# Kernel tuning notes

Hardware: AMD Instinct MI355X
Metric: run time of the kernel (lower is better)

The kernel has to match this reference:

```python
import jax, jax.numpy as jnp
import numpy as np
import math

B, S, D, H = 2, 2048, 512, 8  # batch, seq, d_hidden (= per-head dim here), n_heads


def _rope(x):
    # x: [B, H, S, D]; standard interleaved RoPE with base 10000
    b, h, s, d = x.shape
    inv_freq = 1.0 / (10000.0 ** (jnp.arange(0, d, 2, dtype=jnp.float32) / d))  # [d/2]
    ang = jnp.arange(s, dtype=jnp.float32)[:, None] * inv_freq[None, :]          # [S, d/2]
    cos, sin = jnp.cos(ang), jnp.sin(ang)
    x1, x2 = x[..., 0::2], x[..., 1::2]
    r1 = x1 * cos - x2 * sin
    r2 = x1 * sin + x2 * cos
    return jnp.stack([r1, r2], axis=-1).reshape(b, h, s, d).astype(x.dtype)


def setup_inputs() -> dict:
    key = jax.random.key(0)
    kq, k1, k2, k3, k4 = jax.random.split(key, 5)
    std = 0.02
    return {
        "q": jax.random.normal(kq, (B, S, D), dtype=jnp.float32),
        "W_q": jax.random.normal(k1, (H, D, D), dtype=jnp.float32) * std,
        "W_k": jax.random.normal(k2, (H, D, D), dtype=jnp.float32) * std,
        "W_v": jax.random.normal(k3, (H, D, D), dtype=jnp.float32) * std,
        "W_o": jax.random.normal(k4, (H * D, D), dtype=jnp.float32) * std,
    }


def reference(q, W_q, W_k, W_v, W_o):
    b, s, d = q.shape
    h = W_q.shape[0]
    scale = 1.0 / math.sqrt(d)
    qh = jnp.einsum('bsz,hzd->bhsd', q, W_q)
    kh = jnp.einsum('bsz,hzd->bhsd', q, W_k)
    vh = jnp.einsum('bsz,hzd->bhsd', q, W_v)
    qh = _rope(qh)
    kh = _rope(kh)
    scores = jnp.einsum('bhqd,bhkd->bhqk', qh, kh) * scale
    causal = jnp.triu(jnp.ones((s, s), dtype=bool), k=1)  # True above diagonal
    scores = jnp.where(causal, -jnp.inf, scores)
    probs = jax.nn.softmax(scores, axis=-1)  # dropout is identity in eval
    # NOTE: faithful to the original (transposed) einsum: contracts over the
    # query index z of probs with the sequence index z of v.
    out = jnp.einsum('bhzs,bhzd->bhsd', probs, vh)
    out = out.transpose(0, 2, 1, 3).reshape(b, s, h * d)
    return jnp.einsum('bsz,zd->bsd', out, W_o)
```

## Files before the change

kernel.cpp:

```cpp
#include <hip/hip_runtime.h>
#include <hip/hip_bf16.h>
#include <math.h>
#include <stdint.h>

#define BB 2
#define SS 2048
#define DD 512
#define HH 8
#define NTOK (BB*SS)
#define NQKV (3*HH*DD)
#define BHD  (HH*DD)
#define NBH  (BB*HH)
#define NTILE 136

typedef __attribute__((ext_vector_type(8))) short short8v;
typedef __attribute__((ext_vector_type(4))) float floatx4;

__device__ __forceinline__ unsigned short f2bf(float f) {
  unsigned int u = __builtin_bit_cast(unsigned int, f);
  u = (u + 0x7FFFu + ((u >> 16) & 1u)) >> 16;
  return (unsigned short)u;
}
__device__ __forceinline__ float bf2f(unsigned short s) {
  unsigned int u = ((unsigned int)s) << 16;
  return __builtin_bit_cast(float, u);
}
__device__ __forceinline__ void async16(const void* g, void* l) {
  __builtin_amdgcn_global_load_lds(
      (const __attribute__((address_space(1))) unsigned int*)g,
      (__attribute__((address_space(3))) unsigned int*)l, 16, 0, 0);
}
#define WAITVM(N) asm volatile("s_waitcnt vmcnt(" #N ")" ::: "memory")
#define BAR() __builtin_amdgcn_s_barrier()

__global__ void k_convert_q(const float* __restrict__ q, unsigned short* __restrict__ qbf) {
  int i = (blockIdx.x * 256 + threadIdx.x) * 4;
  const float4 v = *(const float4*)&q[i];
  ushort4 o;
  o.x = f2bf(v.x); o.y = f2bf(v.y); o.z = f2bf(v.z); o.w = f2bf(v.w);
  *(ushort4*)&qbf[i] = o;
}

__global__ void k_rope_tab(float* __restrict__ rope) {
  const int idx = blockIdx.x * 256 + threadIdx.x;
  const int s = idx >> 8, dp = idx & 255;
  const float inv = exp2f(-13.287712379549449f * (1.0f/256.0f) * (float)dp);
  float sn, cs;
  __sincosf((float)s * inv, &sn, &cs);
  rope[(size_t)idx * 2]     = cs;
  rope[(size_t)idx * 2 + 1] = sn;
}

__global__ void k_prep_w(const float* __restrict__ Wq, const float* __restrict__ Wk,
                         const float* __restrict__ Wv, const float* __restrict__ Wo,
                         unsigned short* __restrict__ Wcat, unsigned short* __restrict__ Wot) {
  __shared__ float t[32][33];
  const int z = blockIdx.z;
  const float* in; unsigned short* out; int inLD, outLD;
  float sc = 1.0f;
  if (z < 24) {
    int tsel = z / 8, h = z % 8;
    const float* w = (tsel == 0) ? Wq : (tsel == 1) ? Wk : Wv;
    if (tsel == 0) sc = 0.044194173824159216f;
    in = w + (size_t)h * DD * DD;
    out = Wcat + ((size_t)tsel * BHD + (size_t)h * DD) * DD;
    inLD = DD; outLD = DD;
  } else {
    int k = z - 24;
    in = Wo + (size_t)k * DD * DD;
    out = Wot + (size_t)k * DD;
    inLD = DD; outLD = BHD;
  }
  const int tx = threadIdx.x, ty = threadIdx.y;
  const int bx = blockIdx.x * 32, by = blockIdx.y * 32;
  for (int kk = 0; kk < 4; ++kk)
    t[ty + 8*kk][tx] = in[(size_t)(by + ty + 8*kk) * inLD + bx + tx];
  __syncthreads();
  for (int kk = 0; kk < 4; ++kk)
    out[(size_t)(bx + ty + 8*kk) * outLD + by + tx] = f2bf(t[tx][ty + 8*kk] * sc);
}

__global__ __launch_bounds__(512, 1)
void k_qkv(const unsigned short* __restrict__ Abf, const unsigned short* __restrict__ Bt,
           const float* __restrict__ ropeT,
           unsigned short* __restrict__ Qr, unsigned short* __restrict__ Kr,
           unsigned short* __restrict__ Vt) {
  __shared__ short A_lds[2][2][128*64];
  __shared__ short B_lds[2][2][128*64];
  const int tid = threadIdx.x;
  const int lin2 = (blockIdx.x & 7) * 96 + (blockIdx.x >> 3);
  const int m0 = (lin2 & 15) * 256;
  const int n0 = (lin2 >> 4) * 256;
  const int wave = tid >> 6, lane = tid & 63, qd = lane >> 4, c = lane & 15;
  const int wm = (wave >> 2) * 128;
  const int wn = (wave & 3) * 64;
  const int Ha = wm >> 7;
  const int Hb = wn >> 7;
  const int brw = (wn & 64) + c;
  const int cw = c & 7;
  const int s0q = (qd ^ cw) * 8;
  const int s1q = ((4 | qd) ^ cw) * 8;
  const int trow = tid >> 3;
  const int scol = ((tid & 7) ^ (trow & 7)) * 8;
  const int tlin = tid * 8;
  floatx4 acc[8][4] = {};
  short8v ar[4][2], br0[2][2], br1[2][2];

#define STG_A(T, H) if ((T) < 8) { \
    async16(&Abf[(size_t)(m0 + (H)*128 + trow     ) * 512 + (T)*64 + scol], &A_lds[(T)&1][H][tlin]); \
    async16(&Abf[(size_t)(m0 + (H)*128 + trow + 64) * 512 + (T)*64 + scol], &A_lds[(T)&1][H][tlin + 4096]); }
#define STG_B(T, H) if ((T) < 8) { \
    async16(&Bt [(size_t)(n0 + (H)*128 + trow     ) * 512 + (T)*64 + scol], &B_lds[(T)&1][H][tlin]); \
    async16(&Bt [(size_t)(n0 + (H)*128 + trow + 64) * 512 + (T)*64 + scol], &B_lds[(T)&1][H][tlin + 4096]); }

#define PH(DB, MH, NH, BR, DOA, DOB, STAGE, WAITC) { \
    if (DOA) { \
      _Pragma("unroll") for (int mf = 0; mf < 4; ++mf) { \
        const int ra = ((MH)*64 + mf*16 + c) * 64; \
        ar[mf][0] = *(const short8v*)&A_lds[DB][Ha][ra + s0q]; \
        ar[mf][1] = *(const short8v*)&A_lds[DB][Ha][ra + s1q]; } } \
    if (DOB) { \
      _Pragma("unroll") for (int nf = 0; nf < 2; ++nf) { \
        const int rb = (brw + (NH)*32 + nf*16) * 64; \
        BR[nf][0] = *(const short8v*)&B_lds[DB][Hb][rb + s0q]; \
        BR[nf][1] = *(const short8v*)&B_lds[DB][Hb][rb + s1q]; } } \
    STAGE; \
    BAR(); \
    asm volatile("s_waitcnt lgkmcnt(0)" ::: "memory"); \
    __builtin_amdgcn_s_setprio(1); \
    _Pragma("unroll") for (int mf = 0; mf < 4; ++mf) \
      _Pragma("unroll") for (int nf = 0; nf < 2; ++nf) { \
        acc[(MH)*4+mf][(NH)*2+nf] = __builtin_amdgcn_mfma_f32_16x16x32_bf16(ar[mf][0], BR[nf][0], acc[(MH)*4+mf][(NH)*2+nf], 0, 0, 0); \
        acc[(MH)*4+mf][(NH)*2+nf] = __builtin_amdgcn_mfma_f32_16x16x32_bf16(ar[mf][1], BR[nf][1], acc[(MH)*4+mf][(NH)*2+nf], 0, 0, 0); } \
    __builtin_amdgcn_s_setprio(0); \
    WAITC; \
    BAR(); }

  STG_A(0, 0); STG_A(0, 1); STG_B(0, 0); STG_B(0, 1); STG_A(1, 0);
  WAITVM(2); BAR();

  for (int it = 0; it < 4; ++it) {
    const int t1 = 2*it + 1, t2 = 2*it + 2, t3 = 2*it + 3;
    PH(0, 0, 0, br0, 1, 1, STG_A(t1, 1), ;)
    PH(0, 0, 1, br1, 0, 1, STG_B(t1, 0), ;)
    PH(0, 1, 0, br0, 1, 0, STG_B(t1, 1), ;)
    PH(0, 1, 1, br1, 0, 0, STG_A(t2, 0), if (it < 3) { WAITVM(2); } else { WAITVM(0); })
    PH(1, 0, 0, br0, 1, 1, STG_A(t2, 1), ;)
    PH(1, 0, 1, br1, 0, 1, STG_B(t2, 0), ;)
    PH(1, 1, 0, br0, 1, 0, STG_B(t2, 1), ;)
    PH(1, 1, 1, br1, 0, 0, STG_A(t3, 0), if (it < 3) { WAITVM(2); })
  }
#undef PH
#undef STG_A
#undef STG_B

  const int tsel = n0 >> 12;
  const int h = (n0 >> 9) & 7;
  const int bat = m0 >> 11;
  const int bh = bat * HH + h;
  const int colw = (n0 & 511) + wn;
  if (tsel < 2) {
    unsigned short* dst = (tsel == 0) ? Qr : Kr;
    const int dp0 = (colw >> 1) + (c >> 1);
    const unsigned int sgn = (c & 1) ? 0u : 0x80000000u;
    for (int mi = 0; mi < 8; ++mi) {
      const int mrow = (m0 & 2047) + wm + (mi >> 2)*64 + (mi & 3)*16 + qd*4;
      for (int r = 0; r < 4; ++r) {
        const int s = mrow + r;
        const float2* rp = (const float2*)&ropeT[((size_t)s * 256 + dp0) * 2];
        const size_t ob = ((size_t)bh * SS + s) * DD;
        for (int ni = 0; ni < 4; ++ni) {
          const int dof = (ni >> 1)*32 + (ni & 1)*16;
          const float2 tt = rp[dof >> 1];
          const float v = acc[mi][ni][r];
          float p = __shfl_xor(v, 1, 64);
          p = __builtin_bit_cast(float, __builtin_bit_cast(unsigned int, p) ^ sgn);
          dst[ob + colw + dof + c] = f2bf(fmaf(p, tt.y, v * tt.x));
        }
      }
    }
  } else {
    for (int ni = 0; ni < 4; ++ni) {
      const int d = colw + (ni >> 1)*32 + (ni & 1)*16 + c;
      const size_t vbase = ((size_t)bh * DD + d) * SS;
      for (int mi = 0; mi < 8; ++mi) {
        const int s = (m0 & 2047) + wm + (mi >> 2)*64 + (mi & 3)*16 + qd*4;
        ushort4 u;
        u.x = f2bf(acc[mi][ni][0]); u.y = f2bf(acc[mi][ni][1]);
        u.z = f2bf(acc[mi][ni][2]); u.w = f2bf(acc[mi][ni][3]);
        *(ushort4*)&Vt[vbase + s] = u;
      }
    }
  }
}

__global__ __launch_bounds__(256)
void k_scores(const unsigned short* __restrict__ Qr, const unsigned short* __restrict__ Kr,
              unsigned short* __restrict__ Eg, float* __restrict__ lsum) {
  __shared__ short UN[17408];
  unsigned short* ET = (unsigned short*)UN;
  const int tid = threadIdx.x;
  const int lin = blockIdx.y * 136 + blockIdx.x;
  const int lin2 = (lin & 7) * 272 + (lin >> 3);
  const int bh = lin2 / 136;
  const int t = lin2 % 136;
  int zb = 0;
  while (((zb + 1) * (zb + 2)) / 2 <= t) ++zb;
  const int st = t - (zb * (zb + 1)) / 2;
  const int z0 = zb * 128, s0 = st * 128;
  const int wave = tid >> 6, lane = tid & 63, qd = lane >> 4, c = lane & 15;
  const int wm = (wave >> 1) * 64, wn = (wave & 1) * 64;
  const size_t qb = (size_t)bh * SS * DD;
  floatx4 acc[4][4] = {};
  const int e0 = tid * 8, e1 = e0 + 2048;
  const int r0 = e0 >> 5, c0 = e0 & 31, r1 = e1 >> 5, c1 = e1 & 31;
  auto STAGE = [&](int buf, int k0) {
    short* A = UN + buf * 4096;
    short* B = UN + 8192 + buf * 4096;
    async16(&Qr[qb + (size_t)(z0 + r0) * 512 + k0 + c0], &A[e0]);
    async16(&Qr[qb + (size_t)(z0 + r1) * 512 + k0 + c1], &A[e1]);
    async16(&Kr[qb + (size_t)(s0 + r0) * 512 + k0 + c0], &B[e0]);
    async16(&Kr[qb + (size_t)(s0 + r1) * 512 + k0 + c1], &B[e1]);
  };
  STAGE(0, 0);
  for (int kk = 0; kk < 16; ++kk) {
    const int cur = kk & 1;
    if (kk < 15) { STAGE(cur ^ 1, (kk + 1) * 32); WAITVM(4); }
    else         { WAITVM(0); }
    BAR();
    const short* Asp = UN + cur * 4096;
    const short* Bsp = UN + 8192 + cur * 4096;
    short8v a[4], bfr[4];
    for (int mt = 0; mt < 4; ++mt) a[mt]   = *(const short8v*)&Asp[(wm + mt*16 + c)*32 + qd*8];
    for (int nt = 0; nt < 4; ++nt) bfr[nt] = *(const short8v*)&Bsp[(wn + nt*16 + c)*32 + qd*8];
    for (int mt = 0; mt < 4; ++mt)
      for (int nt = 0; nt < 4; ++nt)
        acc[mt][nt] = __builtin_amdgcn_mfma_f32_16x16x32_bf16(a[mt], bfr[nt], acc[mt][nt], 0, 0, 0);
    BAR();
  }
  const bool diag = (st == zb);
  for (int mt = 0; mt < 4; ++mt) {
    const int zl = wm + mt*16 + qd*4;
    float rs[4] = {0.f, 0.f, 0.f, 0.f};
    for (int nt = 0; nt < 4; ++nt) {
      const int sl = wn + nt*16 + c;
      for (int r = 0; r < 4; ++r) {
        float ev = __expf(acc[mt][nt][r]);
        if (diag && (sl > zl + r)) ev = 0.f;
        acc[mt][nt][r] = ev;
        rs[r] += ev;
      }
    }
    for (int off = 1; off < 16; off <<= 1)
      for (int r = 0; r < 4; ++r) rs[r] += __shfl_xor(rs[r], off, 64);
    if (c == 0)
      for (int r = 0; r < 4; ++r)
        atomicAdd(&lsum[(size_t)bh * SS + z0 + zl + r], rs[r]);
  }
  for (int mt = 0; mt < 4; ++mt) {
    const int zl = wm + mt*16 + qd*4;
    for (int nt = 0; nt < 4; ++nt) {
      const int sl = wn + nt*16 + c;
      ushort4 u;
      u.x = f2bf(acc[mt][nt][0]); u.y = f2bf(acc[mt][nt][1]);
      u.z = f2bf(acc[mt][nt][2]); u.w = f2bf(acc[mt][nt][3]);
      *(ushort4*)&ET[sl * 136 + zl] = u;
    }
  }
  __syncthreads();
  const size_t tb = ((size_t)bh * NTILE + t) * 16384;
  for (int it = 0; it < 8; ++it) {
    const int e = it * 2048 + tid * 8;
    const int row = e >> 7, col = e & 127;
    *(short8v*)&Eg[tb + row * 128 + col] = *(const short8v*)&ET[row * 136 + col];
  }
}

__global__ void k_vscale(unsigned short* __restrict__ Vt, const float* __restrict__ lsum) {
  const int idx = (blockIdx.x * 256 + threadIdx.x) * 8;
  const int z = idx & (SS - 1);
  const int bh = idx >> 20;
  short8v v = *(const short8v*)&Vt[idx];
  const float* lp = &lsum[(size_t)bh * SS + z];
  short8v o;
  for (int i = 0; i < 8; ++i)
    o[i] = (short)f2bf(bf2f((unsigned short)v[i]) / lp[i]);
  *(short8v*)&Vt[idx] = o;
}

__global__ __launch_bounds__(256)
void k_pv(const unsigned short* __restrict__ Eg, const unsigned short* __restrict__ Vs,
          unsigned short* __restrict__ Ocat) {
  __shared__ short Vl[2][2][128*32];
  __shared__ short El[2][2][128*32];
  const int tid = threadIdx.x;
  const int lin = (blockIdx.z * 8 + blockIdx.y) * 4 + blockIdx.x;
  const int lin2 = (lin & 7) * 64 + (lin >> 3);
  const int d0 = (lin2 & 3) * 128;
  const int pr = (lin2 >> 2) & 7;
  const int bh = lin2 >> 5;
  const int bat = bh >> 3, h = bh & 7;
  const int wave = tid >> 6, lane = tid & 63, qd = lane >> 4, c = lane & 15;
  const int wm = (wave >> 1) * 64, wn = (wave & 1) * 64;
  const size_t vbb = (size_t)bh * DD * SS;
  const int e = tid * 8;
  auto STAGE = [&](int buf, int zb, int half, int st) {
    const size_t tb = ((size_t)bh * NTILE + (zb * (zb + 1)) / 2 + st) * 16384;
    const int zbase = zb * 128 + half * 64;
    for (int i = 0; i < 4; ++i) {
      const int ee = e + i * 2048;
      const int kc = ee >> 12, row = (ee >> 5) & 127, col = ee & 31;
      async16(&Vs[vbb + (size_t)(d0 + row) * SS + zbase + kc * 32 + col], &Vl[buf][kc][row * 32 + col]);
    }
    for (int i = 0; i < 4; ++i) {
      const int ee = e + i * 2048;
      const int kc = ee >> 12, row = (ee >> 5) & 127, col = ee & 31;
      async16(&Eg[tb + (size_t)row * 128 + half * 64 + kc * 32 + col], &El[buf][kc][row * 32 + col]);
    }
  };
  for (int sel = 0; sel < 2; ++sel) {
    const int st = sel ? (15 - pr) : pr;
    const int s0 = st * 128;
    floatx4 acc[4][4] = {};
    const int nst = (16 - st) * 2;
    STAGE(0, st, 0, st);
    for (int q2 = 0; q2 < nst; ++q2) {
      const int cur = q2 & 1;
      if (q2 + 1 < nst) { STAGE(cur ^ 1, st + ((q2 + 1) >> 1), (q2 + 1) & 1, st); WAITVM(8); }
      else              { WAITVM(0); }
      BAR();
      for (int kc = 0; kc < 2; ++kc) {
        short8v a[4], b[4];
        for (int dt = 0; dt < 4; ++dt) a[dt] = *(const short8v*)&Vl[cur][kc][(wm + dt*16 + c)*32 + qd*8];
        for (int nt = 0; nt < 4; ++nt) b[nt] = *(const short8v*)&El[cur][kc][(wn + nt*16 + c)*32 + qd*8];
        for (int dt = 0; dt < 4; ++dt)
          for (int nt = 0; nt < 4; ++nt)
            acc[dt][nt] = __builtin_amdgcn_mfma_f32_16x16x32_bf16(a[dt], b[nt], acc[dt][nt], 0, 0, 0);
      }
      BAR();
    }
    for (int nt = 0; nt < 4; ++nt) {
      const int sg = s0 + wn + nt*16 + c;
      const size_t ob = ((size_t)(bat * SS + sg)) * BHD + (size_t)h * DD + d0;
      for (int dt = 0; dt < 4; ++dt) {
        const int dloc = wm + dt*16 + qd*4;
        ushort4 u;
        u.x = f2bf(acc[dt][nt][0]); u.y = f2bf(acc[dt][nt][1]);
        u.z = f2bf(acc[dt][nt][2]); u.w = f2bf(acc[dt][nt][3]);
        *(ushort4*)&Ocat[ob + dloc] = u;
      }
    }
  }
}

__global__ __launch_bounds__(256)
void k_oproj(const unsigned short* __restrict__ Ocat, const unsigned short* __restrict__ Wot,
             float* __restrict__ out) {
  __shared__ short As[2][2][128*32];
  __shared__ short Bs[2][2][128*32];
  const int tid = threadIdx.x;
  const int lin = (blockIdx.z * 4 + blockIdx.y) * 32 + blockIdx.x;
  const int lin2 = (lin & 7) * 64 + (lin >> 3);
  const int m0 = (lin2 & 31) * 128;
  const int rest = lin2 >> 5;
  const int n0 = (rest & 3) * 128;
  const int ks = (rest >> 2) * 1024;
  const int wave = tid >> 6, lane = tid & 63, qd = lane >> 4, c = lane & 15;
  const int wm = (wave >> 1) * 64, wn = (wave & 1) * 64;
  floatx4 acc[4][4] = {};
  const int e0 = tid * 8, e1 = e0 + 2048;
  const int r0 = e0 >> 5, c0 = e0 & 31, r1 = e1 >> 5, c1 = e1 & 31;
  auto STAGE = [&](int buf, int k0) {
    for (int kc = 0; kc < 2; ++kc) {
      const int kk = k0 + kc * 32;
      async16(&Ocat[(size_t)(m0 + r0) * BHD + kk + c0], &As[buf][kc][e0]);
      async16(&Ocat[(size_t)(m0 + r1) * BHD + kk + c1], &As[buf][kc][e1]);
      async16(&Wot [(size_t)(n0 + r0) * BHD + kk + c0], &Bs[buf][kc][e0]);
      async16(&Wot [(size_t)(n0 + r1) * BHD + kk + c1], &Bs[buf][kc][e1]);
    }
  };
  STAGE(0, ks);
  for (int t = 0; t < 16; ++t) {
    const int cur = t & 1;
    if (t < 15) { STAGE(cur ^ 1, ks + (t + 1) * 64); WAITVM(8); }
    else        { WAITVM(0); }
    BAR();
    for (int kc = 0; kc < 2; ++kc) {
      short8v a[4], b[4];
      for (int mt = 0; mt < 4; ++mt) a[mt] = *(const short8v*)&As[cur][kc][(wm + mt*16 + c)*32 + qd*8];
      for (int nt = 0; nt < 4; ++nt) b[nt] = *(const short8v*)&Bs[cur][kc][(wn + nt*16 + c)*32 + qd*8];
      for (int mt = 0; mt < 4; ++mt)
        for (int nt = 0; nt < 4; ++nt)
          acc[mt][nt] = __builtin_amdgcn_mfma_f32_16x16x32_bf16(a[mt], b[nt], acc[mt][nt], 0, 0, 0);
    }
    BAR();
  }
  for (int mt = 0; mt < 4; ++mt) {
    const int m = m0 + wm + mt*16 + qd*4;
    for (int nt = 0; nt < 4; ++nt) {
      const int n = n0 + wn + nt*16 + c;
      for (int r = 0; r < 4; ++r)
        atomicAdd(&out[(size_t)(m + r) * DD + n], acc[mt][nt][r]);
    }
  }
}

extern "C" void kernel_launch(void* const* d_in, const int* in_sizes, int n_in,
                              void* d_out, int out_size, void* d_ws, size_t ws_size,
                              hipStream_t stream) {
  const float* q  = (const float*)d_in[0];
  const float* Wq = (const float*)d_in[1];
  const float* Wk = (const float*)d_in[2];
  const float* Wv = (const float*)d_in[3];
  const float* Wo = (const float*)d_in[4];

  char* base = (char*)d_ws;
  unsigned short* Eg   = (unsigned short*)base;
  unsigned short* qbf  = (unsigned short*)base;
  unsigned short* Wcat = (unsigned short*)(base + 4194304);
  float*          rope = (float*)(base + 16777216);
  char* p = base + 71303168;
  unsigned short* Wot  = (unsigned short*)p; p += 4194304;
  unsigned short* Qr   = (unsigned short*)p;
  unsigned short* Ocat = (unsigned short*)p; p += 33554432;
  unsigned short* Kr   = (unsigned short*)p; p += 33554432;
  unsigned short* Vt   = (unsigned short*)p; p += 33554432;
  float*          lsum = (float*)p;

  hipMemsetAsync(lsum, 0, (size_t)NBH * SS * 4, stream);
  hipMemsetAsync(d_out, 0, (size_t)NTOK * DD * 4, stream);

  k_convert_q<<<NTOK*DD/1024, 256, 0, stream>>>(q, qbf);
  k_rope_tab<<<SS*256/256, 256, 0, stream>>>(rope);
  k_prep_w<<<dim3(16,16,32), dim3(32,8), 0, stream>>>(Wq, Wk, Wv, Wo, Wcat, Wot);
  k_qkv<<<768, 512, 0, stream>>>(qbf, Wcat, rope, Qr, Kr, Vt);
  k_scores<<<dim3(NTILE,16), 256, 0, stream>>>(Qr, Kr, Eg, lsum);
  k_vscale<<<NBH*DD*SS/(256*8), 256, 0, stream>>>(Vt, lsum);
  k_pv<<<dim3(4,8,16), 256, 0, stream>>>(Eg, Vt, Ocat);
  k_oproj<<<dim3(32,4,4), 256, 0, stream>>>(Ocat, Wot, (float*)d_out);
}
```

Baseline: 367.0 us.

## Enlarge score tiles to 256x256 with 8-wave pipelined, swizzled LDS schedule

The scores kernel now computes 256x256 causal tiles with 512 threads instead of 128x128 tiles with 256 threads. It uses a fine-grained phased pipeline with XOR-swizzled LDS, split A/B half-buffers, and s_setprio around the MFMA bursts. The goal is more reuse of Q/K per global load, fewer bank conflicts, and better overlap of loads with MFMA. In exchange, tiles on the diagonal do wasted work on the fully masked upper quarter. Larger blocks with one block per CU also mean fewer blocks in flight, which may hurt occupancy and load balance.

Result: slower. 377.9 us (+3.0%).

```diff
diff --git a/kernel.cpp b/kernel.cpp
--- a/kernel.cpp
+++ b/kernel.cpp
@@ -194,60 +194,93 @@
   }
 }
 
-__global__ __launch_bounds__(256)
+__global__ __launch_bounds__(512, 1)
 void k_scores(const unsigned short* __restrict__ Qr, const unsigned short* __restrict__ Kr,
               unsigned short* __restrict__ Eg, float* __restrict__ lsum) {
-  __shared__ short UN[17408];
-  unsigned short* ET = (unsigned short*)UN;
+  __shared__ short A_lds[2][2][128*64];
+  __shared__ short B_lds[2][2][128*64];
   const int tid = threadIdx.x;
-  const int lin = blockIdx.y * 136 + blockIdx.x;
-  const int lin2 = (lin & 7) * 272 + (lin >> 3);
-  const int bh = lin2 / 136;
-  const int t = lin2 % 136;
-  int zb = 0;
-  while (((zb + 1) * (zb + 2)) / 2 <= t) ++zb;
-  const int st = t - (zb * (zb + 1)) / 2;
-  const int z0 = zb * 128, s0 = st * 128;
+  const int lin2 = (blockIdx.x & 7) * 72 + (blockIdx.x >> 3);
+  const int bh = lin2 / 36;
+  const int t = lin2 % 36;
+  int ZB = 0;
+  while (((ZB + 1) * (ZB + 2)) / 2 <= t) ++ZB;
+  const int ST = t - (ZB * (ZB + 1)) / 2;
+  const int z0 = ZB * 256, s0 = ST * 256;
   const int wave = tid >> 6, lane = tid & 63, qd = lane >> 4, c = lane & 15;
-  const int wm = (wave >> 1) * 64, wn = (wave & 1) * 64;
+  const int wm = (wave >> 2) * 128;
+  const int wn = (wave & 3) * 64;
+  const int Ha = wm >> 7;
+  const int Hb = wn >> 7;
+  const int brw = (wn & 64) + c;
+  const int cw = c & 7;
+  const int s0q = (qd ^ cw) * 8;
+  const int s1q = ((4 | qd) ^ cw) * 8;
+  const int trow = tid >> 3;
+  const int scol = ((tid & 7) ^ (trow & 7)) * 8;
+  const int tlin = tid * 8;
   const size_t qb = (size_t)bh * SS * DD;
-  floatx4 acc[4][4] = {};
-  const int e0 = tid * 8, e1 = e0 + 2048;
-  const int r0 = e0 >> 5, c0 = e0 & 31, r1 = e1 >> 5, c1 = e1 & 31;
-  auto STAGE = [&](int buf, int k0) {
-    short* A = UN + buf * 4096;
-    short* B = UN + 8192 + buf * 4096;
-    async16(&Qr[qb + (size_t)(z0 + r0) * 512 + k0 + c0], &A[e0]);
-    async16(&Qr[qb + (size_t)(z0 + r1) * 512 + k0 + c1], &A[e1]);
-    async16(&Kr[qb + (size_t)(s0 + r0) * 512 + k0 + c0], &B[e0]);
-    async16(&Kr[qb + (size_t)(s0 + r1) * 512 + k0 + c1], &B[e1]);
-  };
-  STAGE(0, 0);
-  for (int kk = 0; kk < 16; ++kk) {
-    const int cur = kk & 1;
-    if (kk < 15) { STAGE(cur ^ 1, (kk + 1) * 32); WAITVM(4); }
-    else         { WAITVM(0); }
-    BAR();
-    const short* Asp = UN + cur * 4096;
-    const short* Bsp = UN + 8192 + cur * 4096;
-    short8v a[4], bfr[4];
-    for (int mt = 0; mt < 4; ++mt) a[mt]   = *(const short8v*)&Asp[(wm + mt*16 + c)*32 + qd*8];
-    for (int nt = 0; nt < 4; ++nt) bfr[nt] = *(const short8v*)&Bsp[(wn + nt*16 + c)*32 + qd*8];
-    for (int mt = 0; mt < 4; ++mt)
-      for (int nt = 0; nt < 4; ++nt)
-        acc[mt][nt] = __builtin_amdgcn_mfma_f32_16x16x32_bf16(a[mt], bfr[nt], acc[mt][nt], 0, 0, 0);
-    BAR();
-  }
-  const bool diag = (st == zb);
-  for (int mt = 0; mt < 4; ++mt) {
-    const int zl = wm + mt*16 + qd*4;
+  floatx4 acc[8][4] = {};
+  short8v ar[4][2], br0[2][2], br1[2][2];
+
+#define STG_A(T, H) if ((T) < 8) { \
+    async16(&Qr[qb + (size_t)(z0 + (H)*128 + trow     ) * 512 + (T)*64 + scol], &A_lds[(T)&1][H][tlin]); \
+    async16(&Qr[qb + (size_t)(z0 + (H)*128 + trow + 64) * 512 + (T)*64 + scol], &A_lds[(T)&1][H][tlin + 4096]); }
+#define STG_B(T, H) if ((T) < 8) { \
+    async16(&Kr[qb + (size_t)(s0 + (H)*128 + trow     ) * 512 + (T)*64 + scol], &B_lds[(T)&1][H][tlin]); \
+    async16(&Kr[qb + (size_t)(s0 + (H)*128 + trow + 64) * 512 + (T)*64 + scol], &B_lds[(T)&1][H][tlin + 4096]); }
+
+#define PH(DB, MH, NH, BR, DOA, DOB, STAGE, WAITC) { \
+    if (DOA) { \
+      _Pragma("unroll") for (int mf = 0; mf < 4; ++mf) { \
+        const int ra = ((MH)*64 + mf*16 + c) * 64; \
+        ar[mf][0] = *(const short8v*)&A_lds[DB][Ha][ra + s0q]; \
+        ar[mf][1] = *(const short8v*)&A_lds[DB][Ha][ra + s1q]; } } \
+    if (DOB) { \
+      _Pragma("unroll") for (int nf = 0; nf < 2; ++nf) { \
+        const int rb = (brw + (NH)*32 + nf*16) * 64; \
+        BR[nf][0] = *(const short8v*)&B_lds[DB][Hb][rb + s0q]; \
+        BR[nf][1] = *(const short8v*)&B_lds[DB][Hb][rb + s1q]; } } \
+    STAGE; \
+    BAR(); \
+    asm volatile("s_waitcnt lgkmcnt(0)" ::: "memory"); \
+    __builtin_amdgcn_s_setprio(1); \
+    _Pragma("unroll") for (int mf = 0; mf < 4; ++mf) \
+      _Pragma("unroll") for (int nf = 0; nf < 2; ++nf) { \
+        acc[(MH)*4+mf][(NH)*2+nf] = __builtin_amdgcn_mfma_f32_16x16x32_bf16(ar[mf][0], BR[nf][0], acc[(MH)*4+mf][(NH)*2+nf], 0, 0, 0); \
+        acc[(MH)*4+mf][(NH)*2+nf] = __builtin_amdgcn_mfma_f32_16x16x32_bf16(ar[mf][1], BR[nf][1], acc[(MH)*4+mf][(NH)*2+nf], 0, 0, 0); } \
+    __builtin_amdgcn_s_setprio(0); \
+    WAITC; \
+    BAR(); }
+
+  STG_A(0, 0); STG_A(0, 1); STG_B(0, 0); STG_B(0, 1); STG_A(1, 0);
+  WAITVM(2); BAR();
+
+  for (int it = 0; it < 4; ++it) {
+    const int t1 = 2*it + 1, t2 = 2*it + 2, t3 = 2*it + 3;
+    PH(0, 0, 0, br0, 1, 1, STG_A(t1, 1), ;)
+    PH(0, 0, 1, br1, 0, 1, STG_B(t1, 0), ;)
+    PH(0, 1, 0, br0, 1, 0, STG_B(t1, 1), ;)
+    PH(0, 1, 1, br1, 0, 0, STG_A(t2, 0), if (it < 3) { WAITVM(2); } else { WAITVM(0); })
+    PH(1, 0, 0, br0, 1, 1, STG_A(t2, 1), ;)
+    PH(1, 0, 1, br1, 0, 1, STG_B(t2, 0), ;)
+    PH(1, 1, 0, br0, 1, 0, STG_B(t2, 1), ;)
+    PH(1, 1, 1, br1, 0, 0, STG_A(t3, 0), if (it < 3) { WAITVM(2); })
+  }
+#undef PH
+#undef STG_A
+#undef STG_B
+
+  const bool diag256 = (ST == ZB);
+  for (int mi = 0; mi < 8; ++mi) {
+    const int zloc = wm + (mi >> 2)*64 + (mi & 3)*16 + qd*4;
     float rs[4] = {0.f, 0.f, 0.f, 0.f};
-    for (int nt = 0; nt < 4; ++nt) {
-      const int sl = wn + nt*16 + c;
+    for (int ni = 0; ni < 4; ++ni) {
+      const int sloc = wn + (ni >> 1)*32 + (ni & 1)*16 + c;
       for (int r = 0; r < 4; ++r) {
-        float ev = __expf(acc[mt][nt][r]);
-        if (diag && (sl > zl + r)) ev = 0.f;
-        acc[mt][nt][r] = ev;
+        float ev = __expf(acc[mi][ni][r]);
+        if (diag256 && (sloc > zloc + r)) ev = 0.f;
+        acc[mi][ni][r] = ev;
         rs[r] += ev;
       }
     }
@@ -255,24 +288,36 @@
       for (int r = 0; r < 4; ++r) rs[r] += __shfl_xor(rs[r], off, 64);
     if (c == 0)
       for (int r = 0; r < 4; ++r)
-        atomicAdd(&lsum[(size_t)bh * SS + z0 + zl + r], rs[r]);
-  }
-  for (int mt = 0; mt < 4; ++mt) {
-    const int zl = wm + mt*16 + qd*4;
-    for (int nt = 0; nt < 4; ++nt) {
-      const int sl = wn + nt*16 + c;
-      ushort4 u;
-      u.x = f2bf(acc[mt][nt][0]); u.y = f2bf(acc[mt][nt][1]);
-      u.z = f2bf(acc[mt][nt][2]); u.w = f2bf(acc[mt][nt][3]);
-      *(ushort4*)&ET[sl * 136 + zl] = u;
-    }
-  }
-  __syncthreads();
-  const size_t tb = ((size_t)bh * NTILE + t) * 16384;
-  for (int it = 0; it < 8; ++it) {
-    const int e = it * 2048 + tid * 8;
-    const int row = e >> 7, col = e & 127;
-    *(short8v*)&Eg[tb + row * 128 + col] = *(const short8v*)&ET[row * 136 + col];
+        atomicAdd(&lsum[(size_t)bh * SS + z0 + zloc + r], rs[r]);
+  }
+
+  for (int sh = 0; sh < 2; ++sh) {
+    BAR();
+    if ((wn >> 7) == sh) {
+      unsigned short* ET = Ha ? (unsigned short*)B_lds : (unsigned short*)A_lds;
+      for (int mi = 0; mi < 8; ++mi) {
+        const int zcol = (mi >> 2)*64 + (mi & 3)*16 + qd*4;
+        for (int ni = 0; ni < 4; ++ni) {
+          const int sl = (wn & 64) + (ni >> 1)*32 + (ni & 1)*16 + c;
+          ushort4 u;
+          u.x = f2bf(acc[mi][ni][0]); u.y = f2bf(acc[mi][ni][1]);
+          u.z = f2bf(acc[mi][ni][2]); u.w = f2bf(acc[mi][ni][3]);
+          *(ushort4*)&ET[sl * 136 + zcol] = u;
+        }
+      }
+    }
+    BAR();
+    for (int zh = 0; zh < 2; ++zh) {
+      const int zb = 2*ZB + zh, stt = 2*ST + sh;
+      if (stt > zb) continue;
+      const unsigned short* ET = zh ? (const unsigned short*)B_lds : (const unsigned short*)A_lds;
+      const size_t tb = ((size_t)bh * NTILE + (zb * (zb + 1)) / 2 + stt) * 16384;
+      for (int itr = 0; itr < 4; ++itr) {
+        const int e = itr * 4096 + tid * 8;
+        const int row = e >> 7, col = e & 127;
+        *(short8v*)&Eg[tb + row * 128 + col] = *(const short8v*)&ET[row * 136 + col];
+      }
+    }
   }
 }
 
@@ -434,7 +479,7 @@
   k_rope_tab<<<SS*256/256, 256, 0, stream>>>(rope);
   k_prep_w<<<dim3(16,16,32), dim3(32,8), 0, stream>>>(Wq, Wk, Wv, Wo, Wcat, Wot);
   k_qkv<<<768, 512, 0, stream>>>(qbf, Wcat, rope, Qr, Kr, Vt);
-  k_scores<<<dim3(NTILE,16), 256, 0, stream>>>(Qr, Kr, Eg, lsum);
+  k_scores<<<576, 512, 0, stream>>>(Qr, Kr, Eg, lsum);
   k_vscale<<<NBH*DD*SS/(256*8), 256, 0, stream>>>(Vt, lsum);
   k_pv<<<dim3(4,8,16), 256, 0, stream>>>(Eg, Vt, Ocat);
   k_oproj<<<dim3(32,4,4), 256, 0, stream>>>(Ocat, Wot, (float*)d_out);
```
